# Kernel optimization log

Measured on AMD Instinct MI355X. Metric: run time of the kernel, lower is better.

Reference implementation:

```python
import jax, jax.numpy as jnp
import numpy as np

COST_BBOX = 1.0
COST_GIOU = 1.0
TOPK = 5


def _make_boxes(key, b, n):
    # valid xyxy boxes in [0,1]: centers + small positive sizes
    kc, ks = jax.random.split(key)
    cxy = jax.random.uniform(kc, (b, n, 2))
    wh = jax.random.uniform(ks, (b, n, 2)) * 0.2 + 0.01
    return jnp.concatenate([cxy - wh / 2, cxy + wh / 2], axis=-1)


def setup_inputs() -> dict:
    key = jax.random.key(0)
    k1, k2, k3, k4 = jax.random.split(key, 4)
    B, NP, NG = 8, 5000, 300
    return {
        "pred_box": _make_boxes(k1, B, NP),
        "pred_obj": jax.random.normal(k3, (B, NP), dtype=jnp.float32),
        "gt_box": _make_boxes(k2, B, NG),
        "gt_obj": jax.random.normal(k4, (B, NG), dtype=jnp.float32),
    }


def pairwise_giou(pb, gb):
    # pb: [B,N,4], gb: [B,M,4] in xyxy -> giou [B,N,M]
    area_p = (pb[..., 2] - pb[..., 0]) * (pb[..., 3] - pb[..., 1])  # [B,N]
    area_g = (gb[..., 2] - gb[..., 0]) * (gb[..., 3] - gb[..., 1])  # [B,M]
    lt = jnp.maximum(pb[:, :, None, :2], gb[:, None, :, :2])  # [B,N,M,2]
    rb = jnp.minimum(pb[:, :, None, 2:], gb[:, None, :, 2:])
    wh = jnp.clip(rb - lt, 0.0)
    inter = wh[..., 0] * wh[..., 1]                                  # [B,N,M]
    union = area_p[:, :, None] + area_g[:, None, :] - inter
    iou = inter / union
    # smallest enclosing box
    lt_e = jnp.minimum(pb[:, :, None, :2], gb[:, None, :, :2])
    rb_e = jnp.maximum(pb[:, :, None, 2:], gb[:, None, :, 2:])
    wh_e = jnp.clip(rb_e - lt_e, 0.0)
    area_e = wh_e[..., 0] * wh_e[..., 1]
    return iou - (area_e - union) / area_e


def cost_matrix(pred_box, gt_box):
    # L1 cdist: [B,N,M]
    cost_bbox = jnp.sum(jnp.abs(pred_box[:, :, None, :] - gt_box[:, None, :, :]), axis=-1)
    cost_giou = 1.0 - pairwise_giou(pred_box, gt_box)
    return COST_BBOX * cost_bbox + COST_GIOU * cost_giou


def reference(pred_box, pred_obj, gt_box, gt_obj):
    C = cost_matrix(pred_box, gt_box)            # [B, N_pred, N_gt]
    Ct = jnp.swapaxes(C, 1, 2)                   # [B, N_gt, N_pred]
    _, idx = jax.lax.top_k(-Ct, TOPK)            # smallest-cost preds per gt: [B, N_gt, TOPK]
    B, M, _ = idx.shape
    matched_pred = idx.reshape(B, M * TOPK).astype(jnp.int32)
    matched_gt = jnp.broadcast_to(jnp.repeat(jnp.arange(M, dtype=jnp.int32), TOPK)[None, :], (B, M * TOPK))
    return matched_pred, matched_gt
```

## Files before the change

### kernel.cpp

```cpp
#include <hip/hip_runtime.h>

#pragma clang fp contract(off)

typedef unsigned long long u64;

#define TOPK 5
#define WAVES 4

#define CE(x, y) do { const u64 _a = (x), _b = (y); const bool _l = _b < _a; \
                      (x) = _l ? _b : _a; (y) = _l ? _a : _b; } while (0)

#define INSERT(nk, k0, k1, k2, k3, k4) do {        \
    const u64 _n = (nk);                           \
    const bool l0 = _n < k0;                       \
    const bool l1 = _n < k1;                       \
    const bool l2 = _n < k2;                       \
    const bool l3 = _n < k3;                       \
    const bool l4 = _n < k4;                       \
    k4 = l4 ? (l3 ? k3 : _n) : k4;                 \
    k3 = l3 ? (l2 ? k2 : _n) : k3;                 \
    k2 = l2 ? (l1 ? k1 : _n) : k2;                 \
    k1 = l1 ? (l0 ? k0 : _n) : k1;                 \
    k0 = l0 ? _n : k0;                             \
} while (0)

__device__ __forceinline__ float fast_div(float a, float b) {
    float r = __builtin_amdgcn_rcpf(b);
    r = fmaf(fmaf(-b, r, 1.0f), r, r);
    float q = a * r;
    q = fmaf(fmaf(-b, q, a), r, q);
    return q;
}

__device__ __forceinline__ u64 eval_rest(const float4 pb, const float cb,
                                         const float4 gb, const float g_area,
                                         const int p) {
    const float area_p = (pb.z - pb.x) * (pb.w - pb.y);
    const float ltx = fmaxf(pb.x, gb.x), lty = fmaxf(pb.y, gb.y);
    const float rbx = fminf(pb.z, gb.z), rby = fminf(pb.w, gb.w);
    const float iw = fmaxf(rbx - ltx, 0.0f), ih = fmaxf(rby - lty, 0.0f);
    const float inter = iw * ih;
    const float uni = area_p + g_area - inter;
    const float iou = fast_div(inter, uni);
    const float ex1 = fminf(pb.x, gb.x), ey1 = fminf(pb.y, gb.y);
    const float ex2 = fmaxf(pb.z, gb.z), ey2 = fmaxf(pb.w, gb.w);
    const float area_e = (ex2 - ex1) * (ey2 - ey1);
    const float giou = iou - fast_div(area_e - uni, area_e);
    const float cost = cb + (1.0f - giou);
    return ((u64)__float_as_uint(cost) << 32) | (unsigned)p;
}

__global__ __launch_bounds__(64 * WAVES) void matcher_topk_kernel(
    const float* __restrict__ pred_box,
    const float* __restrict__ gt_box,
    int* __restrict__ out_pred,
    int* __restrict__ out_gt,
    int B, int NP, int NG)
{
    const int pairsPerB = (NG + 1) >> 1;
    const int tp = blockIdx.x;
    const int b  = tp / pairsPerB;
    const int j  = tp - b * pairsPerB;
    const int m0 = 2 * j;
    const bool has1 = (m0 + 1 < NG);

    const int wid  = threadIdx.x >> 6;
    const int lane = threadIdx.x & 63;
    const int myGt = wid >> 1;
    const int half = wid & 1;

    const float4 gb = ((const float4*)gt_box)[b * NG + (myGt ? (has1 ? m0 + 1 : m0) : m0)];
    const float g_area = (gb.z - gb.x) * (gb.w - gb.y);

    const int NPm1 = NP - 1;
    const int hN   = (NP + 1) >> 1;
    const int start = half ? hN : 0;
    const int pend  = half ? NP : hN;
    int niter = (pend - start + 255) >> 8;
    niter += (niter & 1);

    u64 k0 = ~0ULL, k1 = ~0ULL, k2 = ~0ULL, k3 = ~0ULL, k4 = ~0ULL;
    unsigned thr_u = 0xFFFFFFFFu;

    const float4* pbase = (const float4*)pred_box + (size_t)b * NP;

#define LOADG(it, ra, rb, rc, rd) do {                        \
    const int _i = start + (it) * 256 + lane;                 \
    ra = pbase[min(_i,       NPm1)];                          \
    rb = pbase[min(_i + 64,  NPm1)];                          \
    rc = pbase[min(_i + 128, NPm1)];                          \
    rd = pbase[min(_i + 192, NPm1)];                          \
} while (0)

#define PROC1(pb_, idx_) do {                                            \
    const float _cb = fabsf(pb_.x - gb.x) + fabsf(pb_.y - gb.y)          \
                    + fabsf(pb_.z - gb.z) + fabsf(pb_.w - gb.w);         \
    const bool _valid = (idx_) < pend;                                   \
    const bool _want = (__float_as_uint(_cb) < thr_u) && _valid;         \
    if (__any((int)_want)) {                                             \
        u64 _k = eval_rest(pb_, _cb, gb, g_area, (idx_));                \
        _k = _valid ? _k : ~0ULL;                                        \
        INSERT(_k, k0, k1, k2, k3, k4);                                  \
        thr_u = (unsigned)(k4 >> 32);                                    \
    }                                                                    \
} while (0)

#define PROCG(it, ra, rb, rc, rd) do {                        \
    const int _i0 = start + (it) * 256 + lane;                \
    PROC1(ra, _i0);                                           \
    PROC1(rb, _i0 + 64);                                      \
    PROC1(rc, _i0 + 128);                                     \
    PROC1(rd, _i0 + 192);                                     \
} while (0)

    float4 eA, eB, eC, eD;
    float4 oA, oB, oC, oD;
    LOADG(0, eA, eB, eC, eD);
    LOADG(1, oA, oB, oC, oD);

    const int nOuter = niter >> 1;
    for (int k = 0; k < nOuter; ++k) {
        const int itE = 2 * k;
        PROCG(itE, eA, eB, eC, eD);
        LOADG(itE + 2, eA, eB, eC, eD);
        __builtin_amdgcn_sched_barrier(0);
        PROCG(itE + 1, oA, oB, oC, oD);
        LOADG(itE + 3, oA, oB, oC, oD);
        __builtin_amdgcn_sched_barrier(0);
    }

#undef LOADG
#undef PROC1
#undef PROCG

    #pragma unroll
    for (int off = 1; off < 64; off <<= 1) {
        const u64 b0 = __shfl_xor(k0, off);
        const u64 b1 = __shfl_xor(k1, off);
        const u64 b2 = __shfl_xor(k2, off);
        const u64 b3 = __shfl_xor(k3, off);
        const u64 b4 = __shfl_xor(k4, off);
        u64 m0_ = k0 < b4 ? k0 : b4;
        u64 m1_ = k1 < b3 ? k1 : b3;
        u64 m2_ = k2 < b2 ? k2 : b2;
        u64 m3_ = k3 < b1 ? k3 : b1;
        u64 m4_ = k4 < b0 ? k4 : b0;
        CE(m0_, m1_); CE(m3_, m4_); CE(m2_, m4_); CE(m2_, m3_); CE(m1_, m4_);
        CE(m0_, m3_); CE(m0_, m2_); CE(m1_, m3_); CE(m1_, m2_);
        k0 = m0_; k1 = m1_; k2 = m2_; k3 = m3_; k4 = m4_;
    }

    __shared__ u64 lds[WAVES][TOPK];
    if (lane == 0) {
        lds[wid][0] = k0; lds[wid][1] = k1; lds[wid][2] = k2;
        lds[wid][3] = k3; lds[wid][4] = k4;
    }
    __syncthreads();

    if (threadIdx.x < 2) {
        const int which = threadIdx.x;
        if (which == 0 || has1) {
            const int mm = m0 + which;
            int h0 = 0, h1 = 0;
            const int base = (b * NG + mm) * TOPK;
            #pragma unroll
            for (int r = 0; r < TOPK; ++r) {
                const u64 v0 = lds[which * 2][h0];
                const u64 v1 = lds[which * 2 + 1][h1];
                const bool t = v0 < v1;
                const u64 best = t ? v0 : v1;
                h0 += t; h1 += !t;
                out_pred[base + r] = (int)(unsigned)(best & 0xFFFFFFFFu);
                out_gt[base + r]   = mm;
            }
        }
    }
}

extern "C" void kernel_launch(void* const* d_in, const int* in_sizes, int n_in,
                              void* d_out, int out_size, void* d_ws, size_t ws_size,
                              hipStream_t stream) {
    const float* pred_box = (const float*)d_in[0];
    const float* gt_box   = (const float*)d_in[2];

    const int NP = 5000;
    const int B  = in_sizes[1] / NP;
    const int NG = in_sizes[3] / B;

    int* out_pred = (int*)d_out;
    int* out_gt   = out_pred + B * NG * TOPK;

    const int pairsPerB = (NG + 1) >> 1;
    const int blocks = B * pairsPerB;
    hipLaunchKernelGGL(matcher_topk_kernel, dim3(blocks), dim3(64 * WAVES), 0, stream,
                       pred_box, gt_box, out_pred, out_gt, B, NP, NG);
}
```

Baseline: 39.05 us.

## Replace early-exit insert with branchless sorting-network merge and asm-pipelined loads

Measured after the change: 37.25 us. -4.6%, faster.

```diff
diff --git a/kernel.cpp b/kernel.cpp
--- a/kernel.cpp
+++ b/kernel.cpp
@@ -3,26 +3,13 @@
 #pragma clang fp contract(off)
 
 typedef unsigned long long u64;
+typedef float f4 __attribute__((ext_vector_type(4)));
 
 #define TOPK 5
 #define WAVES 4
 
 #define CE(x, y) do { const u64 _a = (x), _b = (y); const bool _l = _b < _a; \
                       (x) = _l ? _b : _a; (y) = _l ? _a : _b; } while (0)
-
-#define INSERT(nk, k0, k1, k2, k3, k4) do {        \
-    const u64 _n = (nk);                           \
-    const bool l0 = _n < k0;                       \
-    const bool l1 = _n < k1;                       \
-    const bool l2 = _n < k2;                       \
-    const bool l3 = _n < k3;                       \
-    const bool l4 = _n < k4;                       \
-    k4 = l4 ? (l3 ? k3 : _n) : k4;                 \
-    k3 = l3 ? (l2 ? k2 : _n) : k3;                 \
-    k2 = l2 ? (l1 ? k1 : _n) : k2;                 \
-    k1 = l1 ? (l0 ? k0 : _n) : k1;                 \
-    k0 = l0 ? _n : k0;                             \
-} while (0)
 
 __device__ __forceinline__ float fast_div(float a, float b) {
     float r = __builtin_amdgcn_rcpf(b);
@@ -32,10 +19,11 @@
     return q;
 }
 
-__device__ __forceinline__ u64 eval_rest(const float4 pb, const float cb,
-                                         const float4 gb, const float g_area,
-                                         const int p) {
+__device__ __forceinline__ u64 eval_key(const f4 pb, const f4 gb,
+                                        const float g_area, const int p) {
     const float area_p = (pb.z - pb.x) * (pb.w - pb.y);
+    const float cost_bbox = fabsf(pb.x - gb.x) + fabsf(pb.y - gb.y)
+                          + fabsf(pb.z - gb.z) + fabsf(pb.w - gb.w);
     const float ltx = fmaxf(pb.x, gb.x), lty = fmaxf(pb.y, gb.y);
     const float rbx = fminf(pb.z, gb.z), rby = fminf(pb.w, gb.w);
     const float iw = fmaxf(rbx - ltx, 0.0f), ih = fmaxf(rby - lty, 0.0f);
@@ -46,7 +34,7 @@
     const float ex2 = fmaxf(pb.z, gb.z), ey2 = fmaxf(pb.w, gb.w);
     const float area_e = (ex2 - ex1) * (ey2 - ey1);
     const float giou = iou - fast_div(area_e - uni, area_e);
-    const float cost = cb + (1.0f - giou);
+    const float cost = cost_bbox + (1.0f - giou);
     return ((u64)__float_as_uint(cost) << 32) | (unsigned)p;
 }
 
@@ -69,68 +57,82 @@
     const int myGt = wid >> 1;
     const int half = wid & 1;
 
-    const float4 gb = ((const float4*)gt_box)[b * NG + (myGt ? (has1 ? m0 + 1 : m0) : m0)];
+    const f4 gb = ((const f4*)gt_box)[b * NG + (myGt ? (has1 ? m0 + 1 : m0) : m0)];
     const float g_area = (gb.z - gb.x) * (gb.w - gb.y);
 
-    const int NPm1 = NP - 1;
-    const int hN   = (NP + 1) >> 1;
+    const int NPm1  = NP - 1;
+    const int hN    = (NP + 1) >> 1;
     const int start = half ? hN : 0;
     const int pend  = half ? NP : hN;
-    int niter = (pend - start + 255) >> 8;
-    niter += (niter & 1);
+    int ngroups = (pend - start + 255) >> 8;
+    ngroups += (ngroups & 1);
 
     u64 k0 = ~0ULL, k1 = ~0ULL, k2 = ~0ULL, k3 = ~0ULL, k4 = ~0ULL;
-    unsigned thr_u = 0xFFFFFFFFu;
 
-    const float4* pbase = (const float4*)pred_box + (size_t)b * NP;
+    const f4* pbase = (const f4*)pred_box + (size_t)b * NP;
 
-#define LOADG(it, ra, rb, rc, rd) do {                        \
-    const int _i = start + (it) * 256 + lane;                 \
-    ra = pbase[min(_i,       NPm1)];                          \
-    rb = pbase[min(_i + 64,  NPm1)];                          \
-    rc = pbase[min(_i + 128, NPm1)];                          \
-    rd = pbase[min(_i + 192, NPm1)];                          \
+#define GLOAD(g, rA, rB, rC, rD) do {                                        \
+    const int _i = start + (g) * 256 + lane;                                 \
+    const f4* _p0 = pbase + min(_i,       NPm1);                             \
+    const f4* _p1 = pbase + min(_i + 64,  NPm1);                             \
+    const f4* _p2 = pbase + min(_i + 128, NPm1);                             \
+    const f4* _p3 = pbase + min(_i + 192, NPm1);                             \
+    asm volatile("global_load_dwordx4 %0, %1, off" : "=v"(rA) : "v"(_p0));   \
+    asm volatile("global_load_dwordx4 %0, %1, off" : "=v"(rB) : "v"(_p1));   \
+    asm volatile("global_load_dwordx4 %0, %1, off" : "=v"(rC) : "v"(_p2));   \
+    asm volatile("global_load_dwordx4 %0, %1, off" : "=v"(rD) : "v"(_p3));   \
 } while (0)
 
-#define PROC1(pb_, idx_) do {                                            \
-    const float _cb = fabsf(pb_.x - gb.x) + fabsf(pb_.y - gb.y)          \
-                    + fabsf(pb_.z - gb.z) + fabsf(pb_.w - gb.w);         \
-    const bool _valid = (idx_) < pend;                                   \
-    const bool _want = (__float_as_uint(_cb) < thr_u) && _valid;         \
-    if (__any((int)_want)) {                                             \
-        u64 _k = eval_rest(pb_, _cb, gb, g_area, (idx_));                \
-        _k = _valid ? _k : ~0ULL;                                        \
-        INSERT(_k, k0, k1, k2, k3, k4);                                  \
-        thr_u = (unsigned)(k4 >> 32);                                    \
-    }                                                                    \
+#define GWAIT() do {                                   \
+    asm volatile("s_waitcnt vmcnt(4)");                \
+    __builtin_amdgcn_sched_barrier(0);                 \
 } while (0)
 
-#define PROCG(it, ra, rb, rc, rd) do {                        \
-    const int _i0 = start + (it) * 256 + lane;                \
-    PROC1(ra, _i0);                                           \
-    PROC1(rb, _i0 + 64);                                      \
-    PROC1(rc, _i0 + 128);                                     \
-    PROC1(rd, _i0 + 192);                                     \
+#define PROCG(g, rA, rB, rC, rD) do {                                        \
+    const int _i0 = start + (g) * 256 + lane;                                \
+    u64 kA = eval_key(rA, gb, g_area, _i0);                                  \
+    u64 kB = eval_key(rB, gb, g_area, _i0 + 64);                             \
+    u64 kC = eval_key(rC, gb, g_area, _i0 + 128);                            \
+    u64 kD = eval_key(rD, gb, g_area, _i0 + 192);                            \
+    kA = (_i0       < pend) ? kA : ~0ULL;                                    \
+    kB = (_i0 + 64  < pend) ? kB : ~0ULL;                                    \
+    kC = (_i0 + 128 < pend) ? kC : ~0ULL;                                    \
+    kD = (_i0 + 192 < pend) ? kD : ~0ULL;                                    \
+    CE(kA, kB); CE(kC, kD); CE(kA, kC); CE(kB, kD); CE(kB, kC);              \
+    u64 n0 = k0;                                                             \
+    u64 n1 = k1 < kD ? k1 : kD;                                              \
+    u64 n2 = k2 < kC ? k2 : kC;                                              \
+    u64 n3 = k3 < kB ? k3 : kB;                                              \
+    u64 n4 = k4 < kA ? k4 : kA;                                              \
+    CE(n0, n1); CE(n3, n4); CE(n2, n4); CE(n2, n3); CE(n1, n4);              \
+    CE(n0, n3); CE(n0, n2); CE(n1, n3); CE(n1, n2);                          \
+    k0 = n0; k1 = n1; k2 = n2; k3 = n3; k4 = n4;                             \
 } while (0)
 
-    float4 eA, eB, eC, eD;
-    float4 oA, oB, oC, oD;
-    LOADG(0, eA, eB, eC, eD);
-    LOADG(1, oA, oB, oC, oD);
+    f4 eA, eB, eC, eD;
+    f4 oA, oB, oC, oD;
 
-    const int nOuter = niter >> 1;
-    for (int k = 0; k < nOuter; ++k) {
-        const int itE = 2 * k;
-        PROCG(itE, eA, eB, eC, eD);
-        LOADG(itE + 2, eA, eB, eC, eD);
+    GLOAD(0, eA, eB, eC, eD);
+    GLOAD(1, oA, oB, oC, oD);
+
+    for (int g = 0; g < ngroups; g += 2) {
+        GWAIT();
+        PROCG(g, eA, eB, eC, eD);
         __builtin_amdgcn_sched_barrier(0);
-        PROCG(itE + 1, oA, oB, oC, oD);
-        LOADG(itE + 3, oA, oB, oC, oD);
+        GLOAD(g + 2, eA, eB, eC, eD);
+        GWAIT();
+        PROCG(g + 1, oA, oB, oC, oD);
         __builtin_amdgcn_sched_barrier(0);
+        GLOAD(g + 3, oA, oB, oC, oD);
     }
 
-#undef LOADG
-#undef PROC1
+    asm volatile("s_waitcnt vmcnt(0)");
+    __builtin_amdgcn_sched_barrier(0);
+    asm volatile("" :: "v"(eA), "v"(eB), "v"(eC), "v"(eD),
+                       "v"(oA), "v"(oB), "v"(oC), "v"(oD));
+
+#undef GLOAD
+#undef GWAIT
 #undef PROCG
 
     #pragma unroll
```
